# Kernel optimization log

Hardware: AMD Instinct MI355X
Metric: run time of the kernel (lower is better)

The kernel has to match this reference:

```python
import jax, jax.numpy as jnp
import numpy as np

B = 8192
H = 1024            # hidden_size
A = 512             # alphabet_size
S = 2               # sequence_length
D_IN = A * S        # 1024, gate input dim
D1, D2 = H // 2, H // 3   # decoder dims: 512, 341
TEMP = 1.0


def _linear_params(key, out_d, in_d):
    kw, kb = jax.random.split(key)
    lim = 1.0 / np.sqrt(in_d)
    W = jax.random.uniform(kw, (out_d, in_d), minval=-lim, maxval=lim, dtype=jnp.float32)
    b = jax.random.uniform(kb, (out_d,), minval=-lim, maxval=lim, dtype=jnp.float32)
    return W, b


def setup_inputs() -> dict:
    key = jax.random.key(0)
    ks = jax.random.split(key, 16)
    inp = {
        'x': jax.random.normal(ks[0], (B, D_IN), dtype=jnp.float32),
        'h': jax.random.normal(ks[1], (B, H), dtype=jnp.float32),
        'c': jax.random.normal(ks[2], (B, H), dtype=jnp.float32),
    }
    names = [('W_fi', 'b_fi', H, D_IN), ('W_fh', 'b_fh', H, H),
             ('W_ii', 'b_ii', H, D_IN), ('W_ih', 'b_ih', H, H),
             ('W_si', 'b_si', H, D_IN), ('W_sh', 'b_sh', H, H),
             ('W_oi', 'b_oi', H, D_IN), ('W_oh', 'b_oh', H, H),
             ('W_d1', 'b_d1', D1, H), ('W_d2', 'b_d2', D2, D1),
             ('W_d3', 'b_d3', A, D2)]
    for k, (wn, bn, od, idm) in zip(ks[3:3 + len(names)], names):
        W, b = _linear_params(k, od, idm)
        inp[wn] = W
        inp[bn] = b
    return inp


def reference(x, h, c,
              W_fi, b_fi, W_fh, b_fh,
              W_ii, b_ii, W_ih, b_ih,
              W_si, b_si, W_sh, b_sh,
              W_oi, b_oi, W_oh, b_oh,
              W_d1, b_d1, W_d2, b_d2, W_d3, b_d3):
    def lin(v, W, b):
        return v @ W.T + b

    f = jax.nn.sigmoid(lin(x, W_fi, b_fi) + lin(h, W_fh, b_fh))
    i = jax.nn.sigmoid(lin(x, W_ii, b_ii) + lin(h, W_ih, b_ih))
    s = jnp.tanh(lin(x, W_si, b_si) + lin(h, W_sh, b_sh))
    o = jax.nn.sigmoid(lin(x, W_oi, b_oi) + lin(h, W_oh, b_oh))
    c_new = c * f + i * s
    h_new = o * jnp.tanh(c_new)
    d = jnp.tanh(lin(h_new, W_d1, b_d1))
    d = jnp.tanh(lin(d, W_d2, b_d2))
    d = jax.nn.softmax(lin(d, W_d3, b_d3) / TEMP, axis=-1)
    return h_new, d
```

## Files before the change

### kernel.cpp

```cpp
#include <hip/hip_runtime.h>
#include <cstdint>
#include <cstddef>


typedef _Float16 half_t;
typedef _Float16 half8 __attribute__((ext_vector_type(8)));
typedef _Float16 half4v __attribute__((ext_vector_type(4)));
typedef float float4v __attribute__((ext_vector_type(4)));

#define GLD_LDS16(gptr, lptr)                                                  \
  __builtin_amdgcn_global_load_lds(                                            \
      (const __attribute__((address_space(1))) void*)(gptr),                   \
      (__attribute__((address_space(3))) void*)(lptr), 16, 0, 0)

__device__ __forceinline__ float fsig(float x) {
  return 1.0f / (1.0f + __expf(-x));
}
__device__ __forceinline__ float ftanh_(float x) {
  const float e = __expf(2.0f * x);
  return 1.0f - 2.0f / (e + 1.0f);
}

__global__ __launch_bounds__(512, 2) void gemm_gates(const half_t* __restrict__ A,
                                                     const half_t* __restrict__ Bw,
                                                     const float* __restrict__ bias,
                                                     const float* __restrict__ cin,
                                                     float* __restrict__ hout,
                                                     half_t* __restrict__ h2f) {
  constexpr int K = 2048;
  constexpr int NT = 64;
  __shared__ alignas(16) half_t As[3][256 * 32];
  __shared__ alignas(16) half_t Bs[3][256 * 32];
  const int tid = threadIdx.x;
  const int lane = tid & 63;
  const int wave = tid >> 6;
  const int m = lane & 15;
  const int q = lane >> 4;
  const int ks = (q ^ ((m >> 1) & 3)) << 3;
  const int wm = (wave >> 2) << 7;
  const int wn = (wave & 3) << 6;

  const int bid = blockIdx.x;
  const int xcd = bid & 7;
  const int l = bid >> 3;
  const size_t tile_n = (size_t)((xcd << 1) | (l & 1)) << 8;
  const size_t tile_m = (size_t)(l >> 1) << 8;

  const int ci0 = tid, ci1 = tid + 512;
  const int r0 = ci0 >> 2, k0s = (ci0 & 3) ^ ((r0 >> 1) & 3);
  const int r1 = ci1 >> 2, k1s = (ci1 & 3) ^ ((r1 >> 1) & 3);
  const half_t* Ag0 = A + (tile_m + r0) * (size_t)K + k0s * 8;
  const half_t* Ag1 = A + (tile_m + r1) * (size_t)K + k1s * 8;
  const half_t* Bg0 = Bw + (tile_n + r0) * (size_t)K + k0s * 8;
  const half_t* Bg1 = Bw + (tile_n + r1) * (size_t)K + k1s * 8;
  const int p0 = ci0 * 16, p1 = ci1 * 16;

  GLD_LDS16(Ag0, (char*)As[0] + p0);
  GLD_LDS16(Ag1, (char*)As[0] + p1);
  GLD_LDS16(Bg0, (char*)Bs[0] + p0);
  GLD_LDS16(Bg1, (char*)Bs[0] + p1);
  GLD_LDS16(Ag0 + 32, (char*)As[1] + p0);
  GLD_LDS16(Ag1 + 32, (char*)As[1] + p1);
  GLD_LDS16(Bg0 + 32, (char*)Bs[1] + p0);
  GLD_LDS16(Bg1 + 32, (char*)Bs[1] + p1);
  asm volatile("s_waitcnt vmcnt(4)" ::: "memory");
  __builtin_amdgcn_s_barrier();
  __builtin_amdgcn_sched_barrier(0);

  float4v acc[8][4] = {};
  int bc = 0;
  for (int t = 0; t < NT; ++t) {
    const half_t* as = As[bc];
    const half_t* bs = Bs[bc];
    const int bst = (bc + 2 >= 3) ? bc - 1 : bc + 2;
    const size_t koff = (size_t)(t + 2) * 32;
    half8 af[4], bf[4];
#pragma unroll
    for (int i = 0; i < 4; ++i)
      af[i] = *(const half8*)(as + (wm + i * 16 + m) * 32 + ks);
#pragma unroll
    for (int j = 0; j < 4; ++j)
      bf[j] = *(const half8*)(bs + (wn + j * 16 + m) * 32 + ks);
    if (t < NT - 2) {
      GLD_LDS16(Ag0 + koff, (char*)As[bst] + p0);
      GLD_LDS16(Ag1 + koff, (char*)As[bst] + p1);
    }
    __builtin_amdgcn_s_barrier();
    asm volatile("s_waitcnt lgkmcnt(0)" ::: "memory");
    __builtin_amdgcn_sched_barrier(0);
    __builtin_amdgcn_s_setprio(1);
#pragma unroll
    for (int i = 0; i < 4; ++i)
#pragma unroll
      for (int j = 0; j < 4; ++j)
        acc[i][j] = __builtin_amdgcn_mfma_f32_16x16x32_f16(af[i], bf[j],
                                                           acc[i][j], 0, 0, 0);
    __builtin_amdgcn_s_setprio(0);
    __builtin_amdgcn_s_barrier();
    __builtin_amdgcn_sched_barrier(0);
    half8 ag[4];
#pragma unroll
    for (int i = 0; i < 4; ++i)
      ag[i] = *(const half8*)(as + (wm + 64 + i * 16 + m) * 32 + ks);
    if (t < NT - 2) {
      GLD_LDS16(Bg0 + koff, (char*)Bs[bst] + p0);
      GLD_LDS16(Bg1 + koff, (char*)Bs[bst] + p1);
    }
    __builtin_amdgcn_s_barrier();
    asm volatile("s_waitcnt lgkmcnt(0)" ::: "memory");
    __builtin_amdgcn_sched_barrier(0);
    __builtin_amdgcn_s_setprio(1);
#pragma unroll
    for (int i = 0; i < 4; ++i)
#pragma unroll
      for (int j = 0; j < 4; ++j)
        acc[4 + i][j] = __builtin_amdgcn_mfma_f32_16x16x32_f16(
            ag[i], bf[j], acc[4 + i][j], 0, 0, 0);
    __builtin_amdgcn_s_setprio(0);
    if (t < NT - 2) {
      asm volatile("s_waitcnt vmcnt(4)" ::: "memory");
    } else if (t == NT - 2) {
      asm volatile("s_waitcnt vmcnt(0)" ::: "memory");
    }
    __builtin_amdgcn_s_barrier();
    __builtin_amdgcn_sched_barrier(0);
    bc = (bc + 1 == 3) ? 0 : bc + 1;
  }

  const int nwave = (int)tile_n + wn;
  const int u = ((nwave >> 6) << 4) + m;
  const int rtb = (int)((tile_m + wm) >> 4);
  const int ubase = (u >> 5) * 512 + ((u >> 3) & 3) * 128 + (u & 7);
  float bg[4];
#pragma unroll
  for (int g = 0; g < 4; ++g) bg[g] = bias[nwave + g * 16 + m];
#pragma unroll
  for (int i = 0; i < 8; ++i) {
#pragma unroll
    for (int r = 0; r < 4; ++r) {
      const size_t row = tile_m + wm + q * 4 + i * 16 + r;
      const size_t off = row * 1024 + u;
      const float F = fsig(acc[i][0][r] + bg[0]);
      const float I = fsig(acc[i][1][r] + bg[1]);
      const float S = ftanh_(acc[i][2][r] + bg[2]);
      const float O = fsig(acc[i][3][r] + bg[3]);
      const float cn = cin[off] * F + I * S;
      const float hn = O * ftanh_(cn);
      hout[off] = hn;
      h2f[(size_t)(rtb + i) * 16384 + ubase + (q * 4 + r) * 8] = (half_t)hn;
    }
  }
}

__global__ __launch_bounds__(512, 2) void fused_decoder(
    const half_t* __restrict__ h2f,
    const half_t* __restrict__ W1f,
    const float* __restrict__ b1,
    const half_t* __restrict__ W2f,
    const float* __restrict__ b2,
    const half_t* __restrict__ W3f,
    const float* __restrict__ b3,
    float* __restrict__ out) {
  __shared__ alignas(16) half_t A1s[2 * 16384];
  __shared__ alignas(16) half_t A2s[2 * 8192];
  __shared__ alignas(16) half_t A3s[2 * 6144];
  float* LOGL = (float*)A1s;

  const int tid = threadIdx.x;
  const int lane = tid & 63;
  const int w = tid >> 6;
  const int m = lane & 15;
  const int q = lane >> 4;
  const int b = blockIdx.x;

  const half_t* src = h2f + (size_t)b * 32768;
#pragma unroll
  for (int it = 0; it < 8; ++it)
    GLD_LDS16(src + (it * 512 + tid) * 8, (char*)A1s + (it * 512 + tid) * 16);
  asm volatile("s_waitcnt vmcnt(0)" ::: "memory");
  __syncthreads();

  {
    float4v acc[2][4] = {};
    const half_t* w1 = W1f + (size_t)(w * 4) * 16384 + lane * 8;
#pragma unroll 2
    for (int c = 0; c < 32; ++c) {
      half8 wf[4], af[2];
#pragma unroll
      for (int j = 0; j < 4; ++j)
        wf[j] = *(const half8*)(w1 + j * 16384 + c * 512);
#pragma unroll
      for (int rt = 0; rt < 2; ++rt)
        af[rt] = *(const half8*)(A1s + rt * 16384 + c * 512 + q * 128 + m * 8);
#pragma unroll
      for (int rt = 0; rt < 2; ++rt)
#pragma unroll
        for (int j = 0; j < 4; ++j)
          acc[rt][j] = __builtin_amdgcn_mfma_f32_16x16x32_f16(af[rt], wf[j],
                                                              acc[rt][j], 0, 0, 0);
    }
#pragma unroll
    for (int j = 0; j < 4; ++j) {
      const int col = w * 64 + j * 16 + m;
      const float bv = b1[col];
      const int cb = (col >> 5) * 512 + ((col >> 3) & 3) * 128 + (col & 7);
#pragma unroll
      for (int rt = 0; rt < 2; ++rt)
#pragma unroll
        for (int r = 0; r < 4; ++r)
          A2s[rt * 8192 + cb + (q * 4 + r) * 8] = (half_t)ftanh_(acc[rt][j][r] + bv);
    }
  }
  __syncthreads();

  {
    float4v acc[2][3] = {};
    const half_t* w2 = W2f + (size_t)(w * 3) * 8192 + lane * 8;
#pragma unroll 2
    for (int c = 0; c < 16; ++c) {
      half8 wf[3], af[2];
#pragma unroll
      for (int j = 0; j < 3; ++j)
        wf[j] = *(const half8*)(w2 + j * 8192 + c * 512);
#pragma unroll
      for (int rt = 0; rt < 2; ++rt)
        af[rt] = *(const half8*)(A2s + rt * 8192 + c * 512 + q * 128 + m * 8);
#pragma unroll
      for (int rt = 0; rt < 2; ++rt)
#pragma unroll
        for (int j = 0; j < 3; ++j)
          acc[rt][j] = __builtin_amdgcn_mfma_f32_16x16x32_f16(af[rt], wf[j],
                                                              acc[rt][j], 0, 0, 0);
    }
#pragma unroll
    for (int j = 0; j < 3; ++j) {
      const int col = w * 48 + j * 16 + m;
      const float bv = b2[col];
      const int cb = (col >> 5) * 512 + ((col >> 3) & 3) * 128 + (col & 7);
#pragma unroll
      for (int rt = 0; rt < 2; ++rt)
#pragma unroll
        for (int r = 0; r < 4; ++r)
          A3s[rt * 6144 + cb + (q * 4 + r) * 8] = (half_t)ftanh_(acc[rt][j][r] + bv);
    }
  }
  __syncthreads();

  {
    float4v acc[2][4] = {};
    const half_t* w3 = W3f + (size_t)(w * 4) * 6144 + lane * 8;
#pragma unroll 2
    for (int c = 0; c < 12; ++c) {
      half8 wf[4], af[2];
#pragma unroll
      for (int j = 0; j < 4; ++j)
        wf[j] = *(const half8*)(w3 + j * 6144 + c * 512);
#pragma unroll
      for (int rt = 0; rt < 2; ++rt)
        af[rt] = *(const half8*)(A3s + rt * 6144 + c * 512 + q * 128 + m * 8);
#pragma unroll
      for (int rt = 0; rt < 2; ++rt)
#pragma unroll
        for (int j = 0; j < 4; ++j)
          acc[rt][j] = __builtin_amdgcn_mfma_f32_16x16x32_f16(af[rt], wf[j],
                                                              acc[rt][j], 0, 0, 0);
    }
#pragma unroll
    for (int j = 0; j < 4; ++j) {
      const int col = w * 64 + j * 16 + m;
      const float bv = b3[col];
#pragma unroll
      for (int rt = 0; rt < 2; ++rt)
#pragma unroll
        for (int r = 0; r < 4; ++r)
          LOGL[(rt * 16 + q * 4 + r) * 512 + col] = acc[rt][j][r] + bv;
    }
  }
  __syncthreads();

#pragma unroll
  for (int rr = 0; rr < 4; ++rr) {
    const int row = w * 4 + rr;
    const float4v* srcv = (const float4v*)(LOGL + row * 512);
    const float4v v0 = srcv[lane * 2];
    const float4v v1 = srcv[lane * 2 + 1];
    float mx = fmaxf(fmaxf(fmaxf(v0.x, v0.y), fmaxf(v0.z, v0.w)),
                     fmaxf(fmaxf(v1.x, v1.y), fmaxf(v1.z, v1.w)));
#pragma unroll
    for (int off = 32; off > 0; off >>= 1) mx = fmaxf(mx, __shfl_xor(mx, off, 64));
    const float e0 = __expf(v0.x - mx), e1 = __expf(v0.y - mx);
    const float e2 = __expf(v0.z - mx), e3 = __expf(v0.w - mx);
    const float e4 = __expf(v1.x - mx), e5 = __expf(v1.y - mx);
    const float e6 = __expf(v1.z - mx), e7 = __expf(v1.w - mx);
    float sum = ((e0 + e1) + (e2 + e3)) + ((e4 + e5) + (e6 + e7));
#pragma unroll
    for (int off = 32; off > 0; off >>= 1) sum += __shfl_xor(sum, off, 64);
    const float inv = 1.0f / sum;
    float4v o0, o1;
    o0.x = e0 * inv; o0.y = e1 * inv; o0.z = e2 * inv; o0.w = e3 * inv;
    o1.x = e4 * inv; o1.y = e5 * inv; o1.z = e6 * inv; o1.w = e7 * inv;
    float4v* dst = (float4v*)(out + ((size_t)b * 32 + row) * 512);
    dst[lane * 2] = o0;
    dst[lane * 2 + 1] = o1;
  }
}

__global__ void prep_all(const float* __restrict__ x, const float* __restrict__ h,
                         const float* __restrict__ Wfi, const float* __restrict__ Wfh,
                         const float* __restrict__ Wii, const float* __restrict__ Wih,
                         const float* __restrict__ Wsi, const float* __restrict__ Wsh,
                         const float* __restrict__ Woi, const float* __restrict__ Woh,
                         const float* __restrict__ Wd1, const float* __restrict__ Wd2,
                         const float* __restrict__ Wd3, const float* __restrict__ bd2,
                         const float* __restrict__ bfi, const float* __restrict__ bfh,
                         const float* __restrict__ bii, const float* __restrict__ bih,
                         const float* __restrict__ bsi, const float* __restrict__ bsh,
                         const float* __restrict__ boi, const float* __restrict__ boh,
                         half_t* __restrict__ xh, half_t* __restrict__ wall,
                         half_t* __restrict__ WD1, half_t* __restrict__ WD2h,
                         half_t* __restrict__ WD3h, float* __restrict__ BALL,
                         float* __restrict__ BD2) {
  const int bid = blockIdx.x;
  const int tid = threadIdx.x;
  if (bid < 24576) {
    const float* src;
    half_t* dst;
    size_t idx;
    if (bid < 16384) {
      idx = ((size_t)bid * 256 + tid) * 4;
      const size_t bb = idx >> 11;
      const int col = (int)(idx & 2047);
      src = (col < 1024) ? (x + bb * 1024 + col) : (h + bb * 1024 + (col - 1024));
      dst = xh + idx;
    } else {
      idx = ((size_t)(bid - 16384) * 256 + tid) * 4;
      const int n = (int)(idx >> 11);
      const int col = (int)(idx & 2047);
      const int g = (n >> 4) & 3;
      const size_t u = (size_t)(((n >> 6) << 4) | (n & 15));
      const float* Wi = (g == 0) ? Wfi : (g == 1) ? Wii : (g == 2) ? Wsi : Woi;
      const float* Wh = (g == 0) ? Wfh : (g == 1) ? Wih : (g == 2) ? Wsh : Woh;
      src = (col < 1024) ? (Wi + u * 1024 + col) : (Wh + u * 1024 + (col - 1024));
      dst = wall + idx;
    }
    const float4v v = *(const float4v*)src;
    half4v o;
    o.x = (half_t)v.x; o.y = (half_t)v.y; o.z = (half_t)v.z; o.w = (half_t)v.w;
    *(half4v*)dst = o;
    return;
  }
  const int b2i = bid - 24576;
  if (b2i < 512) {
    const size_t i4 = ((size_t)b2i * 256 + tid) * 4;
    const int col = (int)(i4 >> 10);
    const int k0 = (int)(i4 & 1023);
    const float4v v = *(const float4v*)(Wd1 + i4);
    half4v o;
    o.x = (half_t)v.x; o.y = (half_t)v.y; o.z = (half_t)v.z; o.w = (half_t)v.w;
    const size_t fa = (size_t)(col >> 4) * 16384 + (k0 >> 5) * 512 +
                      ((k0 >> 3) & 3) * 128 + (col & 15) * 8 + (k0 & 7);
    *(half4v*)(WD1 + fa) = o;
  } else if (b2i < 704) {
    const size_t i4 = ((size_t)(b2i - 512) * 256 + tid) * 4;
    const int col = (int)(i4 >> 9);
    const int k0 = (int)(i4 & 511);
    half4v o;
    if (col < 341) {
      const float4v v = *(const float4v*)(Wd2 + (size_t)col * 512 + k0);
      o.x = (half_t)v.x; o.y = (half_t)v.y; o.z = (half_t)v.z; o.w = (half_t)v.w;
    } else {
      o.x = (half_t)0.f; o.y = (half_t)0.f; o.z = (half_t)0.f; o.w = (half_t)0.f;
    }
    const size_t fa = (size_t)(col >> 4) * 8192 + (k0 >> 5) * 512 +
                      ((k0 >> 3) & 3) * 128 + (col & 15) * 8 + (k0 & 7);
    *(half4v*)(WD2h + fa) = o;
  } else if (b2i < 896) {
    const size_t i4 = ((size_t)(b2i - 704) * 256 + tid) * 4;
    const int col = (int)(i4 / 384);
    const int k0 = (int)(i4 - (size_t)col * 384);
    half4v o;
    o.x = (k0 + 0 < 341) ? (half_t)Wd3[(size_t)col * 341 + k0 + 0] : (half_t)0.f;
    o.y = (k0 + 1 < 341) ? (half_t)Wd3[(size_t)col * 341 + k0 + 1] : (half_t)0.f;
    o.z = (k0 + 2 < 341) ? (half_t)Wd3[(size_t)col * 341 + k0 + 2] : (half_t)0.f;
    o.w = (k0 + 3 < 341) ? (half_t)Wd3[(size_t)col * 341 + k0 + 3] : (half_t)0.f;
    const size_t fa = (size_t)(col >> 4) * 6144 + (k0 >> 5) * 512 +
                      ((k0 >> 3) & 3) * 128 + (col & 15) * 8 + (k0 & 7);
    *(half4v*)(WD3h + fa) = o;
  } else if (b2i < 912) {
    const int n = (b2i - 896) * 256 + tid;
    const int g = (n >> 4) & 3;
    const int u = ((n >> 6) << 4) | (n & 15);
    const float* bi = (g == 0) ? bfi : (g == 1) ? bii : (g == 2) ? bsi : boi;
    const float* bh = (g == 0) ? bfh : (g == 1) ? bih : (g == 2) ? bsh : boh;
    BALL[n] = bi[u] + bh[u];
  } else {
    const int i = (b2i - 912) * 256 + tid;
    if (i < 384) BD2[i] = (i < 341) ? bd2[i] : 0.0f;
  }
}

extern "C" void kernel_launch(void* const* d_in, const int* in_sizes, int n_in,
                              void* d_out, int out_size, void* d_ws, size_t ws_size,
                              hipStream_t stream) {
  const float* x = (const float*)d_in[0];
  const float* h = (const float*)d_in[1];
  const float* c = (const float*)d_in[2];
  const float* Wfi = (const float*)d_in[3];  const float* bfi = (const float*)d_in[4];
  const float* Wfh = (const float*)d_in[5];  const float* bfh = (const float*)d_in[6];
  const float* Wii = (const float*)d_in[7];  const float* bii = (const float*)d_in[8];
  const float* Wih = (const float*)d_in[9];  const float* bih = (const float*)d_in[10];
  const float* Wsi = (const float*)d_in[11]; const float* bsi = (const float*)d_in[12];
  const float* Wsh = (const float*)d_in[13]; const float* bsh = (const float*)d_in[14];
  const float* Woi = (const float*)d_in[15]; const float* boi = (const float*)d_in[16];
  const float* Woh = (const float*)d_in[17]; const float* boh = (const float*)d_in[18];
  const float* Wd1 = (const float*)d_in[19]; const float* bd1 = (const float*)d_in[20];
  const float* Wd2 = (const float*)d_in[21]; const float* bd2 = (const float*)d_in[22];
  const float* Wd3 = (const float*)d_in[23]; const float* bd3 = (const float*)d_in[24];

  char* ws = (char*)d_ws;
  size_t o = 0;
  auto alloc = [&](size_t bytes) {
    size_t cur = o;
    o += (bytes + 255) & ~(size_t)255;
    return cur;
  };
  half_t* XH   = (half_t*)(ws + alloc((size_t)8192 * 2048 * 2));
  half_t* WALL = (half_t*)(ws + alloc((size_t)4096 * 2048 * 2));
  float*  BALL = (float*)(ws + alloc(4096 * 4));
  half_t* WD1  = (half_t*)(ws + alloc((size_t)512 * 1024 * 2));
  half_t* WD2  = (half_t*)(ws + alloc((size_t)384 * 512 * 2));
  float*  BD2  = (float*)(ws + alloc(384 * 4));
  half_t* WD3  = (half_t*)(ws + alloc((size_t)512 * 384 * 2));
  half_t* H2F  = (half_t*)(ws + alloc((size_t)8192 * 1024 * 2));

  float* h_out = (float*)d_out;
  float* d_outp = (float*)d_out + (size_t)8192 * 1024;

  prep_all<<<25490, 256, 0, stream>>>(x, h, Wfi, Wfh, Wii, Wih, Wsi, Wsh, Woi, Woh,
                                      Wd1, Wd2, Wd3, bd2, bfi, bfh, bii, bih, bsi,
                                      bsh, boi, boh, XH, WALL, WD1, WD2, WD3, BALL,
                                      BD2);

  gemm_gates<<<512, 512, 0, stream>>>(XH, WALL, BALL, c, h_out, H2F);

  fused_decoder<<<256, 512, 0, stream>>>(H2F, WD1, bd1, WD2, BD2, WD3, bd3, d_outp);
}
```

Baseline: 381.5 us.

## Halve decoder rows per block, double grid, and software-pipeline weight loads

The fused decoder now handles 16 batch rows per block instead of 32, so it launches 512 blocks and uses half the shared memory, with launch bounds raised to allow 4 blocks per CU. Each GEMM stage also double-buffers its weight and activation fragment loads so the next chunk is fetched while the current MFMAs run. The aim is more occupancy and latency hiding on a grid that previously covered only 256 CUs once. The cost is that each weight fragment loaded from global/L2 now feeds half as many MFMAs, which doubles total weight traffic, and the tighter register budget may cause spills.

```diff
diff --git a/kernel.cpp b/kernel.cpp
--- a/kernel.cpp
+++ b/kernel.cpp
@@ -152,7 +152,7 @@
   }
 }
 
-__global__ __launch_bounds__(512, 2) void fused_decoder(
+__global__ __launch_bounds__(512, 4) void fused_decoder(
     const half_t* __restrict__ h2f,
     const half_t* __restrict__ W1f,
     const float* __restrict__ b1,
@@ -161,9 +161,9 @@
     const half_t* __restrict__ W3f,
     const float* __restrict__ b3,
     float* __restrict__ out) {
-  __shared__ alignas(16) half_t A1s[2 * 16384];
-  __shared__ alignas(16) half_t A2s[2 * 8192];
-  __shared__ alignas(16) half_t A3s[2 * 6144];
+  __shared__ alignas(16) half_t A1s[16384];
+  __shared__ alignas(16) half_t A2s[8192];
+  __shared__ alignas(16) half_t A3s[6144];
   float* LOGL = (float*)A1s;
 
   const int tid = threadIdx.x;
@@ -173,114 +173,123 @@
   const int q = lane >> 4;
   const int b = blockIdx.x;
 
-  const half_t* src = h2f + (size_t)b * 32768;
-#pragma unroll
-  for (int it = 0; it < 8; ++it)
+  const half_t* src = h2f + (size_t)b * 16384;
+#pragma unroll
+  for (int it = 0; it < 4; ++it)
     GLD_LDS16(src + (it * 512 + tid) * 8, (char*)A1s + (it * 512 + tid) * 16);
   asm volatile("s_waitcnt vmcnt(0)" ::: "memory");
   __syncthreads();
 
   {
-    float4v acc[2][4] = {};
+    float4v acc[4] = {};
     const half_t* w1 = W1f + (size_t)(w * 4) * 16384 + lane * 8;
+    half8 wfA[4], afA;
+#pragma unroll
+    for (int j = 0; j < 4; ++j) wfA[j] = *(const half8*)(w1 + j * 16384);
+    afA = *(const half8*)(A1s + q * 128 + m * 8);
 #pragma unroll 2
-    for (int c = 0; c < 32; ++c) {
-      half8 wf[4], af[2];
-#pragma unroll
-      for (int j = 0; j < 4; ++j)
-        wf[j] = *(const half8*)(w1 + j * 16384 + c * 512);
-#pragma unroll
-      for (int rt = 0; rt < 2; ++rt)
-        af[rt] = *(const half8*)(A1s + rt * 16384 + c * 512 + q * 128 + m * 8);
-#pragma unroll
-      for (int rt = 0; rt < 2; ++rt)
-#pragma unroll
-        for (int j = 0; j < 4; ++j)
-          acc[rt][j] = __builtin_amdgcn_mfma_f32_16x16x32_f16(af[rt], wf[j],
-                                                              acc[rt][j], 0, 0, 0);
-    }
+    for (int c = 0; c < 31; ++c) {
+      half8 wfB[4], afB;
+#pragma unroll
+      for (int j = 0; j < 4; ++j)
+        wfB[j] = *(const half8*)(w1 + j * 16384 + (c + 1) * 512);
+      afB = *(const half8*)(A1s + (c + 1) * 512 + q * 128 + m * 8);
+#pragma unroll
+      for (int j = 0; j < 4; ++j)
+        acc[j] = __builtin_amdgcn_mfma_f32_16x16x32_f16(afA, wfA[j], acc[j], 0, 0, 0);
+#pragma unroll
+      for (int j = 0; j < 4; ++j) wfA[j] = wfB[j];
+      afA = afB;
+    }
+#pragma unroll
+    for (int j = 0; j < 4; ++j)
+      acc[j] = __builtin_amdgcn_mfma_f32_16x16x32_f16(afA, wfA[j], acc[j], 0, 0, 0);
 #pragma unroll
     for (int j = 0; j < 4; ++j) {
       const int col = w * 64 + j * 16 + m;
       const float bv = b1[col];
       const int cb = (col >> 5) * 512 + ((col >> 3) & 3) * 128 + (col & 7);
 #pragma unroll
-      for (int rt = 0; rt < 2; ++rt)
-#pragma unroll
-        for (int r = 0; r < 4; ++r)
-          A2s[rt * 8192 + cb + (q * 4 + r) * 8] = (half_t)ftanh_(acc[rt][j][r] + bv);
+      for (int r = 0; r < 4; ++r)
+        A2s[cb + (q * 4 + r) * 8] = (half_t)ftanh_(acc[j][r] + bv);
     }
   }
   __syncthreads();
 
   {
-    float4v acc[2][3] = {};
+    float4v acc[3] = {};
     const half_t* w2 = W2f + (size_t)(w * 3) * 8192 + lane * 8;
+    half8 wfA[3], afA;
+#pragma unroll
+    for (int j = 0; j < 3; ++j) wfA[j] = *(const half8*)(w2 + j * 8192);
+    afA = *(const half8*)(A2s + q * 128 + m * 8);
 #pragma unroll 2
-    for (int c = 0; c < 16; ++c) {
-      half8 wf[3], af[2];
+    for (int c = 0; c < 15; ++c) {
+      half8 wfB[3], afB;
 #pragma unroll
       for (int j = 0; j < 3; ++j)
-        wf[j] = *(const half8*)(w2 + j * 8192 + c * 512);
-#pragma unroll
-      for (int rt = 0; rt < 2; ++rt)
-        af[rt] = *(const half8*)(A2s + rt * 8192 + c * 512 + q * 128 + m * 8);
-#pragma unroll
-      for (int rt = 0; rt < 2; ++rt)
-#pragma unroll
-        for (int j = 0; j < 3; ++j)
-          acc[rt][j] = __builtin_amdgcn_mfma_f32_16x16x32_f16(af[rt], wf[j],
-                                                              acc[rt][j], 0, 0, 0);
-    }
+        wfB[j] = *(const half8*)(w2 + j * 8192 + (c + 1) * 512);
+      afB = *(const half8*)(A2s + (c + 1) * 512 + q * 128 + m * 8);
+#pragma unroll
+      for (int j = 0; j < 3; ++j)
+        acc[j] = __builtin_amdgcn_mfma_f32_16x16x32_f16(afA, wfA[j], acc[j], 0, 0, 0);
+#pragma unroll
+      for (int j = 0; j < 3; ++j) wfA[j] = wfB[j];
+      afA = afB;
+    }
+#pragma unroll
+    for (int j = 0; j < 3; ++j)
+      acc[j] = __builtin_amdgcn_mfma_f32_16x16x32_f16(afA, wfA[j], acc[j], 0, 0, 0);
 #pragma unroll
     for (int j = 0; j < 3; ++j) {
       const int col = w * 48 + j * 16 + m;
       const float bv = b2[col];
       const int cb = (col >> 5) * 512 + ((col >> 3) & 3) * 128 + (col & 7);
 #pragma unroll
-      for (int rt = 0; rt < 2; ++rt)
-#pragma unroll
-        for (int r = 0; r < 4; ++r)
-          A3s[rt * 6144 + cb + (q * 4 + r) * 8] = (half_t)ftanh_(acc[rt][j][r] + bv);
+      for (int r = 0; r < 4; ++r)
+        A3s[cb + (q * 4 + r) * 8] = (half_t)ftanh_(acc[j][r] + bv);
     }
   }
   __syncthreads();
 
   {
-    float4v acc[2][4] = {};
+    float4v acc[4] = {};
     const half_t* w3 = W3f + (size_t)(w * 4) * 6144 + lane * 8;
+    half8 wfA[4], afA;
+#pragma unroll
+    for (int j = 0; j < 4; ++j) wfA[j] = *(const half8*)(w3 + j * 6144);
+    afA = *(const half8*)(A3s + q * 128 + m * 8);
 #pragma unroll 2
-    for (int c = 0; c < 12; ++c) {
-      half8 wf[4], af[2];
-#pragma unroll
-      for (int j = 0; j < 4; ++j)
-        wf[j] = *(const half8*)(w3 + j * 6144 + c * 512);
-#pragma unroll
-      for (int rt = 0; rt < 2; ++rt)
-        af[rt] = *(const half8*)(A3s + rt * 6144 + c * 512 + q * 128 + m * 8);
-#pragma unroll
-      for (int rt = 0; rt < 2; ++rt)
-#pragma unroll
-        for (int j = 0; j < 4; ++j)
-          acc[rt][j] = __builtin_amdgcn_mfma_f32_16x16x32_f16(af[rt], wf[j],
-                                                              acc[rt][j], 0, 0, 0);
-    }
+    for (int c = 0; c < 11; ++c) {
+      half8 wfB[4], afB;
+#pragma unroll
+      for (int j = 0; j < 4; ++j)
+        wfB[j] = *(const half8*)(w3 + j * 6144 + (c + 1) * 512);
+      afB = *(const half8*)(A3s + (c + 1) * 512 + q * 128 + m * 8);
+#pragma unroll
+      for (int j = 0; j < 4; ++j)
+        acc[j] = __builtin_amdgcn_mfma_f32_16x16x32_f16(afA, wfA[j], acc[j], 0, 0, 0);
+#pragma unroll
+      for (int j = 0; j < 4; ++j) wfA[j] = wfB[j];
+      afA = afB;
+    }
+#pragma unroll
+    for (int j = 0; j < 4; ++j)
+      acc[j] = __builtin_amdgcn_mfma_f32_16x16x32_f16(afA, wfA[j], acc[j], 0, 0, 0);
 #pragma unroll
     for (int j = 0; j < 4; ++j) {
       const int col = w * 64 + j * 16 + m;
       const float bv = b3[col];
 #pragma unroll
-      for (int rt = 0; rt < 2; ++rt)
-#pragma unroll
-        for (int r = 0; r < 4; ++r)
-          LOGL[(rt * 16 + q * 4 + r) * 512 + col] = acc[rt][j][r] + bv;
+      for (int r = 0; r < 4; ++r)
+        LOGL[(q * 4 + r) * 512 + col] = acc[j][r] + bv;
     }
   }
   __syncthreads();
 
 #pragma unroll
-  for (int rr = 0; rr < 4; ++rr) {
-    const int row = w * 4 + rr;
+  for (int rr = 0; rr < 2; ++rr) {
+    const int row = w * 2 + rr;
     const float4v* srcv = (const float4v*)(LOGL + row * 512);
     const float4v v0 = srcv[lane * 2];
     const float4v v1 = srcv[lane * 2 + 1];
@@ -299,7 +308,7 @@
     float4v o0, o1;
     o0.x = e0 * inv; o0.y = e1 * inv; o0.z = e2 * inv; o0.w = e3 * inv;
     o1.x = e4 * inv; o1.y = e5 * inv; o1.z = e6 * inv; o1.w = e7 * inv;
-    float4v* dst = (float4v*)(out + ((size_t)b * 32 + row) * 512);
+    float4v* dst = (float4v*)(out + ((size_t)b * 16 + row) * 512);
     dst[lane * 2] = o0;
     dst[lane * 2 + 1] = o1;
   }
@@ -443,5 +452,5 @@
 
   gemm_gates<<<512, 512, 0, stream>>>(XH, WALL, BALL, c, h_out, H2F);
 
-  fused_decoder<<<256, 512, 0, stream>>>(H2F, WD1, bd1, WD2, BD2, WD3, bd3, d_outp);
-}
+  fused_decoder<<<512, 512, 0, stream>>>(H2F, WD1, bd1, WD2, BD2, WD3, bd3, d_outp);
+}
```

After: 405.1 us. 6.2% more time.
